# Performance work log

Measured on AMD Instinct MI355X. Metric: run time of the kernel, lower is better.

## Reference

```python
import jax, jax.numpy as jnp
import numpy as np


def setup_inputs() -> dict:
    key = jax.random.key(0)
    ks = jax.random.split(key, 5)
    B, Lq, Lk, KD, E, VD = 2, 1024, 1024, 128, 128, 128
    return {
        "query": jax.random.normal(ks[0], (B, Lq, KD), dtype=jnp.float32),
        "key": jax.random.normal(ks[1], (B, Lk, KD), dtype=jnp.float32),
        "value": jax.random.normal(ks[2], (B, Lk, VD), dtype=jnp.float32),
        "vT": jax.random.normal(ks[3], (E,), dtype=jnp.float32) * (1.0 / np.sqrt(E)),
        "weight": jax.random.normal(ks[4], (E, 2 * KD), dtype=jnp.float32) * (1.0 / np.sqrt(2 * KD)),
    }


def reference(query, key, value, vT, weight):
    # Additive (Bahdanau) attention: score(i,j) = vT . tanh(W @ concat(q_i, k_j))
    kdim = query.shape[-1]
    Wq = weight[:, :kdim]   # [E, kdim] acts on query half of concat
    Wk = weight[:, kdim:]   # [E, kdim] acts on key half
    qp = jnp.einsum("bqd,ed->bqe", query, Wq)   # [B, Lq, E]
    kp = jnp.einsum("bkd,ed->bke", key, Wk)     # [B, Lk, E]
    # broadcast-add replaces the explicit concat+linear: [B, Lq, Lk, E]
    h = jnp.tanh(qp[:, :, None, :] + kp[:, None, :, :])
    scores = jnp.einsum("bqke,e->bqk", h, vT)    # [B, Lq, Lk]
    attn = jax.nn.softmax(scores, axis=-1)
    return jnp.einsum("bqk,bkv->bqv", attn, value)  # [B, Lq, Vd]
```

## Files before the change

kernel.cpp:

```cpp
#include <hip/hip_runtime.h>

#define CSC 2.88539008177792681f

typedef float v2f __attribute__((ext_vector_type(2)));

__device__ __forceinline__ float fast_exp2(float x) {
  return __builtin_amdgcn_exp2f(x);
}
__device__ __forceinline__ float fast_rcp(float x) {
  return __builtin_amdgcn_rcpf(x);
}
__device__ __forceinline__ v2f vfma(v2f a, v2f b, v2f c) {
  return __builtin_elementwise_fma(a, b, c);
}
__device__ __forceinline__ v2f vsplat(float s) {
  v2f r;
  r[0] = s;
  r[1] = s;
  return r;
}
__device__ __forceinline__ float rdlane(float v, int l) {
  return __int_as_float(__builtin_amdgcn_readlane(__float_as_int(v), l));
}

__global__ __launch_bounds__(256) void proj_kernel(
    const float* __restrict__ query, const float* __restrict__ key,
    const float* __restrict__ weight, float* __restrict__ Eq,
    float* __restrict__ EkT) {
  __shared__ __align__(16) float rows[16][128];
  __shared__ __align__(16) float tile[16][128];
  int blk = blockIdx.x;
  bool isK = blk >= 128;
  const float* src = isK ? key : query;
  int woff = isK ? 128 : 0;
  int row0 = (isK ? blk - 128 : blk) * 16;
  int tid = threadIdx.x;
#pragma unroll
  for (int i = 0; i < 8; ++i) {
    int f = i * 256 + tid;
    rows[f >> 7][f & 127] = src[(size_t)row0 * 128 + f];
  }
  __syncthreads();
  int e = tid & 127;
  int rh = (tid >> 7) * 8;
  float acc[8];
#pragma unroll
  for (int i = 0; i < 8; ++i) acc[i] = 0.f;
  const float4* wrow =
      reinterpret_cast<const float4*>(weight + (size_t)e * 256 + woff);
#pragma unroll 4
  for (int d4 = 0; d4 < 32; ++d4) {
    float4 wv = wrow[d4];
#pragma unroll
    for (int i = 0; i < 8; ++i) {
      float4 rv = *reinterpret_cast<const float4*>(&rows[rh + i][d4 * 4]);
      acc[i] = fmaf(rv.x, wv.x, acc[i]);
      acc[i] = fmaf(rv.y, wv.y, acc[i]);
      acc[i] = fmaf(rv.z, wv.z, acc[i]);
      acc[i] = fmaf(rv.w, wv.w, acc[i]);
    }
  }
  if (!isK) {
#pragma unroll
    for (int i = 0; i < 8; ++i)
      Eq[(size_t)(row0 + rh + i) * 128 + e] = fast_exp2(CSC * acc[i]);
  } else {
#pragma unroll
    for (int i = 0; i < 8; ++i) tile[rh + i][e] = fast_exp2(CSC * acc[i]);
    __syncthreads();
    int eo = tid >> 1;
    int rseg = (tid & 1) * 8;
    float4 v0 = make_float4(tile[rseg + 0][eo], tile[rseg + 1][eo],
                            tile[rseg + 2][eo], tile[rseg + 3][eo]);
    float4 v1 = make_float4(tile[rseg + 4][eo], tile[rseg + 5][eo],
                            tile[rseg + 6][eo], tile[rseg + 7][eo]);
    float* dst = EkT + (size_t)eo * 2048 + row0 + rseg;
    *reinterpret_cast<float4*>(dst) = v0;
    *reinterpret_cast<float4*>(dst + 4) = v1;
  }
}

__device__ __forceinline__ void quad4(const float4 eq, const float4 vt, v2f ek0,
                                      v2f ek1, v2f ek2, v2f ek3, v2f& acc) {
  v2f one = vsplat(1.f);
  v2f A0 = vfma(vsplat(eq.x), ek0, one);
  v2f A1 = vfma(vsplat(eq.y), ek1, one);
  v2f A2 = vfma(vsplat(eq.z), ek2, one);
  v2f A3 = vfma(vsplat(eq.w), ek3, one);
  v2f P01 = A0 * A1;
  v2f P23 = A2 * A3;
  v2f t01 = vfma(vsplat(vt.x), A1, vsplat(vt.y) * A0);
  v2f t23 = vfma(vsplat(vt.z), A3, vsplat(vt.w) * A2);
  v2f num = vfma(t23, P01, t01 * P23);
  v2f den = P01 * P23;
  v2f r;
  r[0] = fast_rcp(den[0]);
  r[1] = fast_rcp(den[1]);
  acc = vfma(num, r, acc);
}

__global__ __launch_bounds__(512, 2) void attn_kernel(
    const float* __restrict__ Eq, const float* __restrict__ EkT,
    const float* __restrict__ vT, const float* __restrict__ value,
    float* __restrict__ out) {
  __shared__ __align__(16) float sc[8][1024];
  __shared__ __align__(16) v2f pout[8][8][64];
  __shared__ float denom[8];

  int tid = threadIdx.x;
  int lane = tid & 63;
  int w = tid >> 6;
  int b = blockIdx.x >> 7;
  int q0 = (blockIdx.x & 127) * 8;

  {
    const float* ekp = EkT + (size_t)b * 1024 + 2 * tid;
    const float* eqbase = Eq + (size_t)(b * 1024 + q0) * 128;
    v2f acc[8];
#pragma unroll
    for (int q = 0; q < 8; ++q) acc[q] = vsplat(0.f);
    for (int e = 0; e < 128; e += 4) {
      v2f ek0 = *reinterpret_cast<const v2f*>(ekp + (size_t)(e + 0) * 2048);
      v2f ek1 = *reinterpret_cast<const v2f*>(ekp + (size_t)(e + 1) * 2048);
      v2f ek2 = *reinterpret_cast<const v2f*>(ekp + (size_t)(e + 2) * 2048);
      v2f ek3 = *reinterpret_cast<const v2f*>(ekp + (size_t)(e + 3) * 2048);
      float4 vt4 = *reinterpret_cast<const float4*>(vT + e);
#pragma unroll
      for (int q = 0; q < 8; ++q) {
        float4 eq4 =
            *reinterpret_cast<const float4*>(eqbase + (size_t)q * 128 + e);
        quad4(eq4, vt4, ek0, ek1, ek2, ek3, acc[q]);
      }
    }
#pragma unroll
    for (int q = 0; q < 8; ++q)
      *reinterpret_cast<v2f*>(&sc[q][2 * tid]) = acc[q];
  }
  __syncthreads();

  {
    float sum = 0.f;
#pragma unroll
    for (int i = 0; i < 16; ++i) {
      int k = i * 64 + lane;
      float p = fast_exp2(-CSC * sc[w][k]);
      sc[w][k] = p;
      sum += p;
    }
#pragma unroll
    for (int off = 32; off; off >>= 1) sum += __shfl_xor(sum, off);
    if (lane == 0) denom[w] = sum;
  }
  __syncthreads();

  {
    v2f acc[8];
#pragma unroll
    for (int q = 0; q < 8; ++q) acc[q] = vsplat(0.f);
    const v2f* vp = reinterpret_cast<const v2f*>(value) +
                    (size_t)b * 1024 * 64 + lane;
#pragma unroll
    for (int half = 0; half < 2; ++half) {
      int kb = w * 128 + half * 64;
      float pr[8];
#pragma unroll
      for (int q = 0; q < 8; ++q) pr[q] = sc[q][kb + lane];
#pragma unroll
      for (int kk = 0; kk < 64; ++kk) {
        v2f vv = vp[(size_t)(kb + kk) * 64];
#pragma unroll
        for (int q = 0; q < 8; ++q)
          acc[q] = vfma(vsplat(rdlane(pr[q], kk)), vv, acc[q]);
      }
    }
#pragma unroll
    for (int q = 0; q < 8; ++q) pout[w][q][lane] = acc[q];
  }
  __syncthreads();

  {
    int q = tid >> 6;
    v2f r = pout[0][q][lane];
#pragma unroll
    for (int ww = 1; ww < 8; ++ww) r = r + pout[ww][q][lane];
    float inv = fast_rcp(denom[q]);
    r[0] *= inv;
    r[1] *= inv;
    reinterpret_cast<v2f*>(out)[(size_t)(b * 1024 + q0 + q) * 64 + lane] = r;
  }
}

extern "C" void kernel_launch(void* const* d_in, const int* in_sizes, int n_in,
                              void* d_out, int out_size, void* d_ws,
                              size_t ws_size, hipStream_t stream) {
  const float* query = (const float*)d_in[0];
  const float* key = (const float*)d_in[1];
  const float* value = (const float*)d_in[2];
  const float* vT = (const float*)d_in[3];
  const float* weight = (const float*)d_in[4];
  float* out = (float*)d_out;
  float* Eq = (float*)d_ws;
  float* EkT = Eq + 2048 * 128;
  proj_kernel<<<256, 256, 0, stream>>>(query, key, weight, Eq, EkT);
  attn_kernel<<<256, 512, 0, stream>>>(Eq, EkT, vT, value, out);
}
```

Baseline: 48.17 us.

## Use 1024-thread attention blocks, fuse exp into scoring, read probs from LDS

The attention kernel now launches 1024 threads per block. Each half of the block scores 4 of the 8 queries, and the exponentials and per-wave partial sums are computed right after scoring instead of in a separate softmax pass. In the PV stage each of 16 waves covers 64 keys and reads probabilities as float4 from shared memory instead of broadcasting them with readlane. This adds parallelism and removes one LDS pass, but raises register pressure under the 1024-thread launch bound and the shared-memory footprint for the 16-way partial outputs.

```diff
diff --git a/kernel.cpp b/kernel.cpp
--- a/kernel.cpp
+++ b/kernel.cpp
@@ -18,9 +18,6 @@
   r[0] = s;
   r[1] = s;
   return r;
-}
-__device__ __forceinline__ float rdlane(float v, int l) {
-  return __int_as_float(__builtin_amdgcn_readlane(__float_as_int(v), l));
 }
 
 __global__ __launch_bounds__(256) void proj_kernel(
@@ -99,12 +96,13 @@
   acc = vfma(num, r, acc);
 }
 
-__global__ __launch_bounds__(512, 2) void attn_kernel(
+__global__ __launch_bounds__(1024, 4) void attn_kernel(
     const float* __restrict__ Eq, const float* __restrict__ EkT,
     const float* __restrict__ vT, const float* __restrict__ value,
     float* __restrict__ out) {
   __shared__ __align__(16) float sc[8][1024];
-  __shared__ __align__(16) v2f pout[8][8][64];
+  __shared__ __align__(16) v2f pout[16][8][64];
+  __shared__ float wsum[16][4];
   __shared__ float denom[8];
 
   int tid = threadIdx.x;
@@ -112,13 +110,17 @@
   int w = tid >> 6;
   int b = blockIdx.x >> 7;
   int q0 = (blockIdx.x & 127) * 8;
+  int half = tid >> 9;
+  int kp = tid & 511;
+  int qh = half * 4;
 
   {
-    const float* ekp = EkT + (size_t)b * 1024 + 2 * tid;
-    const float* eqbase = Eq + (size_t)(b * 1024 + q0) * 128;
-    v2f acc[8];
-#pragma unroll
-    for (int q = 0; q < 8; ++q) acc[q] = vsplat(0.f);
+    const float* ekp = EkT + (size_t)b * 1024 + 2 * kp;
+    const float* eqb = Eq + (size_t)(b * 1024 + q0 + qh) * 128;
+    v2f acc[4];
+#pragma unroll
+    for (int q = 0; q < 4; ++q) acc[q] = vsplat(0.f);
+#pragma unroll 2
     for (int e = 0; e < 128; e += 4) {
       v2f ek0 = *reinterpret_cast<const v2f*>(ekp + (size_t)(e + 0) * 2048);
       v2f ek1 = *reinterpret_cast<const v2f*>(ekp + (size_t)(e + 1) * 2048);
@@ -126,63 +128,65 @@
       v2f ek3 = *reinterpret_cast<const v2f*>(ekp + (size_t)(e + 3) * 2048);
       float4 vt4 = *reinterpret_cast<const float4*>(vT + e);
 #pragma unroll
-      for (int q = 0; q < 8; ++q) {
+      for (int q = 0; q < 4; ++q) {
         float4 eq4 =
-            *reinterpret_cast<const float4*>(eqbase + (size_t)q * 128 + e);
+            *reinterpret_cast<const float4*>(eqb + (size_t)q * 128 + e);
         quad4(eq4, vt4, ek0, ek1, ek2, ek3, acc[q]);
       }
     }
 #pragma unroll
-    for (int q = 0; q < 8; ++q)
-      *reinterpret_cast<v2f*>(&sc[q][2 * tid]) = acc[q];
+    for (int q = 0; q < 4; ++q) {
+      v2f p;
+      p[0] = fast_exp2(-CSC * acc[q][0]);
+      p[1] = fast_exp2(-CSC * acc[q][1]);
+      *reinterpret_cast<v2f*>(&sc[qh + q][2 * kp]) = p;
+      float s = p[0] + p[1];
+#pragma unroll
+      for (int off = 32; off; off >>= 1) s += __shfl_xor(s, off);
+      if (lane == 0) wsum[w][q] = s;
+    }
   }
   __syncthreads();
+  if (tid < 8) {
+    int base = (tid >> 2) * 8;
+    float s = 0.f;
+#pragma unroll
+    for (int ww = 0; ww < 8; ++ww) s += wsum[base + ww][tid & 3];
+    denom[tid] = s;
+  }
 
   {
-    float sum = 0.f;
-#pragma unroll
-    for (int i = 0; i < 16; ++i) {
-      int k = i * 64 + lane;
-      float p = fast_exp2(-CSC * sc[w][k]);
-      sc[w][k] = p;
-      sum += p;
-    }
-#pragma unroll
-    for (int off = 32; off; off >>= 1) sum += __shfl_xor(sum, off);
-    if (lane == 0) denom[w] = sum;
+    int kb = w * 64;
+    v2f acc2[8];
+#pragma unroll
+    for (int q = 0; q < 8; ++q) acc2[q] = vsplat(0.f);
+    const v2f* vp =
+        reinterpret_cast<const v2f*>(value) + (size_t)b * 1024 * 64 + lane;
+#pragma unroll 2
+    for (int kk = 0; kk < 64; kk += 4) {
+      v2f vv0 = vp[(size_t)(kb + kk + 0) * 64];
+      v2f vv1 = vp[(size_t)(kb + kk + 1) * 64];
+      v2f vv2 = vp[(size_t)(kb + kk + 2) * 64];
+      v2f vv3 = vp[(size_t)(kb + kk + 3) * 64];
+#pragma unroll
+      for (int q = 0; q < 8; ++q) {
+        float4 pp = *reinterpret_cast<const float4*>(&sc[q][kb + kk]);
+        acc2[q] = vfma(vsplat(pp.x), vv0, acc2[q]);
+        acc2[q] = vfma(vsplat(pp.y), vv1, acc2[q]);
+        acc2[q] = vfma(vsplat(pp.z), vv2, acc2[q]);
+        acc2[q] = vfma(vsplat(pp.w), vv3, acc2[q]);
+      }
+    }
+#pragma unroll
+    for (int q = 0; q < 8; ++q) pout[w][q][lane] = acc2[q];
   }
   __syncthreads();
 
-  {
-    v2f acc[8];
-#pragma unroll
-    for (int q = 0; q < 8; ++q) acc[q] = vsplat(0.f);
-    const v2f* vp = reinterpret_cast<const v2f*>(value) +
-                    (size_t)b * 1024 * 64 + lane;
-#pragma unroll
-    for (int half = 0; half < 2; ++half) {
-      int kb = w * 128 + half * 64;
-      float pr[8];
-#pragma unroll
-      for (int q = 0; q < 8; ++q) pr[q] = sc[q][kb + lane];
-#pragma unroll
-      for (int kk = 0; kk < 64; ++kk) {
-        v2f vv = vp[(size_t)(kb + kk) * 64];
-#pragma unroll
-        for (int q = 0; q < 8; ++q)
-          acc[q] = vfma(vsplat(rdlane(pr[q], kk)), vv, acc[q]);
-      }
-    }
-#pragma unroll
-    for (int q = 0; q < 8; ++q) pout[w][q][lane] = acc[q];
-  }
-  __syncthreads();
-
-  {
+  if (tid < 512) {
     int q = tid >> 6;
     v2f r = pout[0][q][lane];
 #pragma unroll
-    for (int ww = 1; ww < 8; ++ww) r = r + pout[ww][q][lane];
+    for (int ww = 1; ww < 16; ++ww) r = r + pout[ww][q][lane];
     float inv = fast_rcp(denom[q]);
     r[0] *= inv;
     r[1] *= inv;
@@ -202,5 +206,5 @@
   float* Eq = (float*)d_ws;
   float* EkT = Eq + 2048 * 128;
   proj_kernel<<<256, 256, 0, stream>>>(query, key, weight, Eq, EkT);
-  attn_kernel<<<256, 512, 0, stream>>>(Eq, EkT, vT, value, out);
-}
+  attn_kernel<<<256, 1024, 0, stream>>>(Eq, EkT, vT, value, out);
+}
```

Result: slower. 55.44 us (+15.1%).

## Split attention over key quarters with partial sums and a combine kernel

Applied to the files above, without the earlier changes.

The attention kernel now splits the 1024 keys into four 256-key chunks, so each block covers 8 queries by 256 keys and the grid grows from 256 to 1024 blocks. Per-block unnormalized outputs and partial softmax denominators go to workspace, and a new combine kernel sums them and normalizes. This relies on the score bound, with no max subtraction, to keep partial sums exact. The PV loop now reads probabilities from shared memory with float4 loads instead of using readlane broadcasts. The aim is more parallelism and occupancy on the GPU, at the cost of an extra launch and workspace traffic.

```diff
diff --git a/kernel.cpp b/kernel.cpp
--- a/kernel.cpp
+++ b/kernel.cpp
@@ -18,9 +18,6 @@
   r[0] = s;
   r[1] = s;
   return r;
-}
-__device__ __forceinline__ float rdlane(float v, int l) {
-  return __int_as_float(__builtin_amdgcn_readlane(__float_as_int(v), l));
 }
 
 __global__ __launch_bounds__(256) void proj_kernel(
@@ -99,57 +96,59 @@
   acc = vfma(num, r, acc);
 }
 
-__global__ __launch_bounds__(512, 2) void attn_kernel(
+__global__ __launch_bounds__(512, 4) void attn_kernel(
     const float* __restrict__ Eq, const float* __restrict__ EkT,
     const float* __restrict__ vT, const float* __restrict__ value,
-    float* __restrict__ out) {
-  __shared__ __align__(16) float sc[8][1024];
+    float* __restrict__ pblk, float* __restrict__ dsum) {
+  __shared__ __align__(16) float sc[8][256];
   __shared__ __align__(16) v2f pout[8][8][64];
-  __shared__ float denom[8];
 
   int tid = threadIdx.x;
   int lane = tid & 63;
   int w = tid >> 6;
-  int b = blockIdx.x >> 7;
-  int q0 = (blockIdx.x & 127) * 8;
+  int bi = blockIdx.x;
+  int b = bi >> 9;
+  int qg = (bi >> 2) & 127;
+  int kh = bi & 3;
+  int q0 = qg * 8;
+  int koff = kh * 256;
+  int kp = tid & 127;
+  int qp = tid >> 7;
 
   {
-    const float* ekp = EkT + (size_t)b * 1024 + 2 * tid;
-    const float* eqbase = Eq + (size_t)(b * 1024 + q0) * 128;
-    v2f acc[8];
-#pragma unroll
-    for (int q = 0; q < 8; ++q) acc[q] = vsplat(0.f);
+    const float* ekp = EkT + (size_t)b * 1024 + koff + 2 * kp;
+    const float* eqb = Eq + (size_t)(b * 1024 + q0 + qp * 2) * 128;
+    v2f accA = vsplat(0.f), accB = vsplat(0.f);
+#pragma unroll 2
     for (int e = 0; e < 128; e += 4) {
       v2f ek0 = *reinterpret_cast<const v2f*>(ekp + (size_t)(e + 0) * 2048);
       v2f ek1 = *reinterpret_cast<const v2f*>(ekp + (size_t)(e + 1) * 2048);
       v2f ek2 = *reinterpret_cast<const v2f*>(ekp + (size_t)(e + 2) * 2048);
       v2f ek3 = *reinterpret_cast<const v2f*>(ekp + (size_t)(e + 3) * 2048);
       float4 vt4 = *reinterpret_cast<const float4*>(vT + e);
-#pragma unroll
-      for (int q = 0; q < 8; ++q) {
-        float4 eq4 =
-            *reinterpret_cast<const float4*>(eqbase + (size_t)q * 128 + e);
-        quad4(eq4, vt4, ek0, ek1, ek2, ek3, acc[q]);
-      }
-    }
-#pragma unroll
-    for (int q = 0; q < 8; ++q)
-      *reinterpret_cast<v2f*>(&sc[q][2 * tid]) = acc[q];
-  }
-  __syncthreads();
-
-  {
-    float sum = 0.f;
-#pragma unroll
-    for (int i = 0; i < 16; ++i) {
-      int k = i * 64 + lane;
-      float p = fast_exp2(-CSC * sc[w][k]);
-      sc[w][k] = p;
-      sum += p;
-    }
-#pragma unroll
-    for (int off = 32; off; off >>= 1) sum += __shfl_xor(sum, off);
-    if (lane == 0) denom[w] = sum;
+      float4 eqA = *reinterpret_cast<const float4*>(eqb + e);
+      float4 eqB = *reinterpret_cast<const float4*>(eqb + 128 + e);
+      quad4(eqA, vt4, ek0, ek1, ek2, ek3, accA);
+      quad4(eqB, vt4, ek0, ek1, ek2, ek3, accB);
+    }
+    v2f pA, pB;
+    pA[0] = fast_exp2(-CSC * accA[0]);
+    pA[1] = fast_exp2(-CSC * accA[1]);
+    pB[0] = fast_exp2(-CSC * accB[0]);
+    pB[1] = fast_exp2(-CSC * accB[1]);
+    *reinterpret_cast<v2f*>(&sc[qp * 2 + 0][2 * kp]) = pA;
+    *reinterpret_cast<v2f*>(&sc[qp * 2 + 1][2 * kp]) = pB;
+    float sA = pA[0] + pA[1];
+    float sB = pB[0] + pB[1];
+#pragma unroll
+    for (int off = 32; off; off >>= 1) {
+      sA += __shfl_xor(sA, off);
+      sB += __shfl_xor(sB, off);
+    }
+    if (lane == 0) {
+      dsum[(size_t)bi * 16 + (qp * 2 + 0) * 2 + (w & 1)] = sA;
+      dsum[(size_t)bi * 16 + (qp * 2 + 1) * 2 + (w & 1)] = sB;
+    }
   }
   __syncthreads();
 
@@ -157,20 +156,22 @@
     v2f acc[8];
 #pragma unroll
     for (int q = 0; q < 8; ++q) acc[q] = vsplat(0.f);
+    int kb = w * 32;
     const v2f* vp = reinterpret_cast<const v2f*>(value) +
-                    (size_t)b * 1024 * 64 + lane;
-#pragma unroll
-    for (int half = 0; half < 2; ++half) {
-      int kb = w * 128 + half * 64;
-      float pr[8];
-#pragma unroll
-      for (int q = 0; q < 8; ++q) pr[q] = sc[q][kb + lane];
-#pragma unroll
-      for (int kk = 0; kk < 64; ++kk) {
-        v2f vv = vp[(size_t)(kb + kk) * 64];
-#pragma unroll
-        for (int q = 0; q < 8; ++q)
-          acc[q] = vfma(vsplat(rdlane(pr[q], kk)), vv, acc[q]);
+                    ((size_t)b * 1024 + koff + kb) * 64 + lane;
+#pragma unroll 2
+    for (int k4 = 0; k4 < 8; ++k4) {
+      v2f vv0 = vp[(size_t)(k4 * 4 + 0) * 64];
+      v2f vv1 = vp[(size_t)(k4 * 4 + 1) * 64];
+      v2f vv2 = vp[(size_t)(k4 * 4 + 2) * 64];
+      v2f vv3 = vp[(size_t)(k4 * 4 + 3) * 64];
+#pragma unroll
+      for (int q = 0; q < 8; ++q) {
+        float4 pp = *reinterpret_cast<const float4*>(&sc[q][kb + k4 * 4]);
+        acc[q] = vfma(vsplat(pp.x), vv0, acc[q]);
+        acc[q] = vfma(vsplat(pp.y), vv1, acc[q]);
+        acc[q] = vfma(vsplat(pp.z), vv2, acc[q]);
+        acc[q] = vfma(vsplat(pp.w), vv3, acc[q]);
       }
     }
 #pragma unroll
@@ -183,11 +184,33 @@
     v2f r = pout[0][q][lane];
 #pragma unroll
     for (int ww = 1; ww < 8; ++ww) r = r + pout[ww][q][lane];
-    float inv = fast_rcp(denom[q]);
-    r[0] *= inv;
-    r[1] *= inv;
-    reinterpret_cast<v2f*>(out)[(size_t)(b * 1024 + q0 + q) * 64 + lane] = r;
-  }
+    *reinterpret_cast<v2f*>(pblk + (size_t)bi * 1024 + q * 128 + 2 * lane) = r;
+  }
+}
+
+__global__ __launch_bounds__(512) void combine_kernel(
+    const float* __restrict__ pblk, const float* __restrict__ dsum,
+    float* __restrict__ out) {
+  int g = blockIdx.x * 512 + threadIdx.x;
+  int row = g >> 6;
+  int c = g & 63;
+  int b = row >> 10;
+  int qg = (row >> 3) & 127;
+  int q = row & 7;
+  int bi0 = b * 512 + qg * 4;
+  v2f r = vsplat(0.f);
+  float d = 0.f;
+#pragma unroll
+  for (int kh = 0; kh < 4; ++kh) {
+    r = r + *reinterpret_cast<const v2f*>(
+                pblk + (size_t)(bi0 + kh) * 1024 + q * 128 + 2 * c);
+    d += dsum[(size_t)(bi0 + kh) * 16 + q * 2 + 0] +
+         dsum[(size_t)(bi0 + kh) * 16 + q * 2 + 1];
+  }
+  float inv = fast_rcp(d);
+  r[0] *= inv;
+  r[1] *= inv;
+  *reinterpret_cast<v2f*>(out + (size_t)row * 128 + 2 * c) = r;
 }
 
 extern "C" void kernel_launch(void* const* d_in, const int* in_sizes, int n_in,
@@ -200,7 +223,10 @@
   const float* weight = (const float*)d_in[4];
   float* out = (float*)d_out;
   float* Eq = (float*)d_ws;
-  float* EkT = Eq + 2048 * 128;
+  float* EkT = Eq + 262144;
+  float* pblk = EkT + 262144;
+  float* dsum = pblk + 1048576;
   proj_kernel<<<256, 256, 0, stream>>>(query, key, weight, Eq, EkT);
-  attn_kernel<<<256, 512, 0, stream>>>(Eq, EkT, vT, value, out);
-}
+  attn_kernel<<<1024, 512, 0, stream>>>(Eq, EkT, vT, value, pblk, dsum);
+  combine_kernel<<<256, 512, 0, stream>>>(pblk, dsum, out);
+}
```

New measurement: 70.23 us. +45.8%, slower.
